# Performance work log

Measured on AMD Instinct MI355X. Metric: run time of the kernel, lower is better.

Reference implementation:

```python
import jax, jax.numpy as jnp
import numpy as np

N_CLS = 20
EMBED_DIM = 256


def setup_inputs() -> dict:
    key = jax.random.key(0)
    k1, k2 = jax.random.split(key)
    patch_embed = jax.random.normal(k1, (64, 4096, EMBED_DIM), dtype=jnp.float32)
    # xavier_uniform init for codebook: bound = sqrt(6/(fan_in+fan_out))
    bound = float(np.sqrt(6.0 / (N_CLS + EMBED_DIM)))
    codebook = jax.random.uniform(k2, (N_CLS, EMBED_DIM), dtype=jnp.float32,
                                  minval=-bound, maxval=bound)
    return {"patch_embed": patch_embed, "codebook": codebook}


def reference(patch_embed, codebook):
    # scores: (B, n_cls, N) = codebook (c,d) . patch_embed (b,n,d)
    attn = jnp.einsum('cd,bnd->bcn', codebook, patch_embed)
    attn = jax.nn.softmax(attn, axis=-1)
    # attn_patch: (B, n_cls, D)
    return jnp.einsum('bcn,bnd->bcd', attn, patch_embed)
```

## Files before the change

### kernel.cpp

```cpp
#include <hip/hip_runtime.h>
#include <cmath>

#define BATCH 64
#define NTOK  4096
#define DIM   256
#define NCLS  20
#define TILE  16
#define XPAD  65
#define CQ    17

#define GLOAD_LDS16(gp, lp) \
  __builtin_amdgcn_global_load_lds((const __attribute__((address_space(1))) void*)(gp), \
                                   (__attribute__((address_space(3))) void*)(lp), 16, 0, 0)

__device__ __forceinline__ float wave_sum64(float v) {
  #pragma unroll
  for (int m = 32; m >= 1; m >>= 1) v += __shfl_xor(v, m, 64);
  return v;
}

__global__ __launch_bounds__(256, 4) void patch_attn_chunk(
    const float* __restrict__ patch, const float* __restrict__ codebook,
    float* __restrict__ o_ws, float* __restrict__ l_ws, int nch) {
  __shared__ float4 Xs[TILE * XPAD];
  __shared__ float4 CBs[NCLS * 4 * CQ];
  __shared__ float4 Ps4[4 * TILE];
  __shared__ float  Ps1[4 * TILE];

  const int tid  = threadIdx.x;
  const int w    = tid >> 6;
  const int lane = tid & 63;
  const int r    = lane & 15;
  const int q    = lane >> 4;
  const int b    = blockIdx.x / nch;
  const int ch   = blockIdx.x - b * nch;
  const int rows = NTOK / nch;
  const int ntiles = rows / TILE;
  const float4* Xg  = (const float4*)patch + ((size_t)b * NTOK + (size_t)ch * rows) * (DIM / 4);
  const float4* cb4 = (const float4*)codebook;
  const int c0 = __builtin_amdgcn_readfirstlane(w * 5);

  #pragma unroll
  for (int idx = tid; idx < NCLS * 64; idx += 256) {
    int cls = idx >> 6, rest = idx & 63;
    int qq = rest >> 4, i = rest & 15;
    CBs[cls * (4 * CQ) + qq * CQ + i] = cb4[idx];
  }

  float4 o[5];
  float l_run[5];
  #pragma unroll
  for (int j = 0; j < 5; ++j) {
    o[j] = make_float4(0.f, 0.f, 0.f, 0.f);
    l_run[j] = 0.f;
  }

  for (int t = 0; t < ntiles; ++t) {
    const float4* srcT = Xg + (size_t)t * TILE * (DIM / 4);
    #pragma unroll
    for (int i = 0; i < 4; ++i) {
      const int n = i * 4 + w;
      GLOAD_LDS16(srcT + n * (DIM / 4) + lane, &Xs[n * XPAD + lane]);
    }
    __syncthreads();

    float s[5] = {0.f, 0.f, 0.f, 0.f, 0.f};
    {
      const int xb  = r * XPAD + q * 16;
      const int cbb = q * CQ;
      #pragma unroll 8
      for (int cbi = 0; cbi < 16; ++cbi) {
        float4 x = Xs[xb + cbi];
        #pragma unroll
        for (int j = 0; j < 5; ++j) {
          float4 cv = CBs[(c0 + j) * (4 * CQ) + cbb + cbi];
          s[j] = fmaf(x.x, cv.x, s[j]);
          s[j] = fmaf(x.y, cv.y, s[j]);
          s[j] = fmaf(x.z, cv.z, s[j]);
          s[j] = fmaf(x.w, cv.w, s[j]);
        }
      }
    }
    float p[5];
    #pragma unroll
    for (int j = 0; j < 5; ++j) {
      s[j] += __shfl_xor(s[j], 16, 64);
      s[j] += __shfl_xor(s[j], 32, 64);
      p[j] = __expf(s[j]);
      l_run[j] += p[j];
    }

    if (lane < 16) {
      Ps4[w * TILE + r] = make_float4(p[0], p[1], p[2], p[3]);
      Ps1[w * TILE + r] = p[4];
    }

    #pragma unroll 8
    for (int n = 0; n < TILE; ++n) {
      float4 x  = Xs[n * XPAD + lane];
      float4 pv = Ps4[w * TILE + n];
      float  p4 = Ps1[w * TILE + n];
      o[0].x = fmaf(pv.x, x.x, o[0].x); o[0].y = fmaf(pv.x, x.y, o[0].y);
      o[0].z = fmaf(pv.x, x.z, o[0].z); o[0].w = fmaf(pv.x, x.w, o[0].w);
      o[1].x = fmaf(pv.y, x.x, o[1].x); o[1].y = fmaf(pv.y, x.y, o[1].y);
      o[1].z = fmaf(pv.y, x.z, o[1].z); o[1].w = fmaf(pv.y, x.w, o[1].w);
      o[2].x = fmaf(pv.z, x.x, o[2].x); o[2].y = fmaf(pv.z, x.y, o[2].y);
      o[2].z = fmaf(pv.z, x.z, o[2].z); o[2].w = fmaf(pv.z, x.w, o[2].w);
      o[3].x = fmaf(pv.w, x.x, o[3].x); o[3].y = fmaf(pv.w, x.y, o[3].y);
      o[3].z = fmaf(pv.w, x.z, o[3].z); o[3].w = fmaf(pv.w, x.w, o[3].w);
      o[4].x = fmaf(p4,   x.x, o[4].x); o[4].y = fmaf(p4,   x.y, o[4].y);
      o[4].z = fmaf(p4,   x.z, o[4].z); o[4].w = fmaf(p4,   x.w, o[4].w);
    }
    __syncthreads();
  }

  const size_t base = (size_t)(b * nch + ch) * NCLS + c0;
  float4* og = (float4*)o_ws;
  #pragma unroll
  for (int j = 0; j < 5; ++j) og[(base + j) * (DIM / 4) + lane] = o[j];
  #pragma unroll
  for (int j = 0; j < 5; ++j) l_run[j] = 0.25f * wave_sum64(l_run[j]);
  if (lane == 0) {
    #pragma unroll
    for (int j = 0; j < 5; ++j) l_ws[base + j] = l_run[j];
  }
}

__global__ __launch_bounds__(256) void patch_attn_combine(
    const float* __restrict__ o_ws, const float* __restrict__ l_ws,
    float* __restrict__ out, int nch) {
  const int bc = blockIdx.x;
  const int b = bc / NCLS;
  const int c = bc - b * NCLS;
  const int d = threadIdx.x;

  float lg = 0.f, acc = 0.f;
  for (int ch = 0; ch < nch; ++ch) {
    size_t idx = ((size_t)b * nch + ch) * NCLS + c;
    lg  += l_ws[idx];
    acc += o_ws[idx * DIM + d];
  }
  out[(size_t)bc * DIM + d] = acc / lg;
}

extern "C" void kernel_launch(void* const* d_in, const int* in_sizes, int n_in,
                              void* d_out, int out_size, void* d_ws, size_t ws_size,
                              hipStream_t stream) {
  const float* patch = (const float*)d_in[0];
  const float* cbk   = (const float*)d_in[1];
  float* out = (float*)d_out;

  int nch = 16;
  while (nch > 1 && (size_t)BATCH * nch * NCLS * (DIM + 1) * sizeof(float) > ws_size) nch >>= 1;

  float* o_ws = (float*)d_ws;
  float* l_ws = o_ws + (size_t)BATCH * nch * NCLS * DIM;

  patch_attn_chunk<<<dim3(BATCH * nch), dim3(256), 0, stream>>>(patch, cbk, o_ws, l_ws, nch);
  patch_attn_combine<<<dim3(BATCH * NCLS), dim3(256), 0, stream>>>(o_ws, l_ws, out, nch);
}
```

Before: 390.1 us.

## Restructure chunk kernel with 64-row XOR-swizzled tiles and per-thread full-class accumulators

Grows the row tile from 16 to 64 and stores rows unpadded in LDS with an XOR swizzle to avoid bank conflicts. Each lane now computes full-dimension dot products for one row, reading codebook values straight from global memory, so the cross-lane shuffle reduction goes away. In the second GEMM each thread owns one output dimension and accumulates all 20 classes, with probabilities shared through LDS. The chunk count drops from 16 to 8 and occupancy is lowered to 2 blocks, trading register pressure and fewer barriers per row for fewer blocks in flight.

```diff
diff --git a/kernel.cpp b/kernel.cpp
--- a/kernel.cpp
+++ b/kernel.cpp
@@ -5,9 +5,7 @@
 #define NTOK  4096
 #define DIM   256
 #define NCLS  20
-#define TILE  16
-#define XPAD  65
-#define CQ    17
+#define RT    64
 
 #define GLOAD_LDS16(gp, lp) \
   __builtin_amdgcn_global_load_lds((const __attribute__((address_space(1))) void*)(gp), \
@@ -19,110 +17,116 @@
   return v;
 }
 
-__global__ __launch_bounds__(256, 4) void patch_attn_chunk(
+__global__ __launch_bounds__(256, 2) void patch_attn_chunk(
     const float* __restrict__ patch, const float* __restrict__ codebook,
     float* __restrict__ o_ws, float* __restrict__ l_ws, int nch) {
-  __shared__ float4 Xs[TILE * XPAD];
-  __shared__ float4 CBs[NCLS * 4 * CQ];
-  __shared__ float4 Ps4[4 * TILE];
-  __shared__ float  Ps1[4 * TILE];
+  __shared__ float4 Xs[RT * (DIM / 4)];
+  __shared__ float  Ps[RT * NCLS];
 
   const int tid  = threadIdx.x;
   const int w    = tid >> 6;
   const int lane = tid & 63;
-  const int r    = lane & 15;
-  const int q    = lane >> 4;
   const int b    = blockIdx.x / nch;
   const int ch   = blockIdx.x - b * nch;
   const int rows = NTOK / nch;
-  const int ntiles = rows / TILE;
+  const int ntiles = rows / RT;
   const float4* Xg  = (const float4*)patch + ((size_t)b * NTOK + (size_t)ch * rows) * (DIM / 4);
   const float4* cb4 = (const float4*)codebook;
   const int c0 = __builtin_amdgcn_readfirstlane(w * 5);
 
+  float o[NCLS];
   #pragma unroll
-  for (int idx = tid; idx < NCLS * 64; idx += 256) {
-    int cls = idx >> 6, rest = idx & 63;
-    int qq = rest >> 4, i = rest & 15;
-    CBs[cls * (4 * CQ) + qq * CQ + i] = cb4[idx];
-  }
+  for (int c = 0; c < NCLS; ++c) o[c] = 0.f;
+  float l0 = 0.f, l1 = 0.f, l2 = 0.f, l3 = 0.f, l4 = 0.f;
 
-  float4 o[5];
-  float l_run[5];
+  const int rx = lane & 7;
+  const float4* xp[8];
   #pragma unroll
-  for (int j = 0; j < 5; ++j) {
-    o[j] = make_float4(0.f, 0.f, 0.f, 0.f);
-    l_run[j] = 0.f;
-  }
+  for (int k = 0; k < 8; ++k) xp[k] = &Xs[lane * (DIM / 4) + (k ^ rx)];
+
+  const float* XsF = (const float*)Xs;
+  const int f4d = tid >> 2, fsub = tid & 3;
+  const float* xbp[8];
+  #pragma unroll
+  for (int k = 0; k < 8; ++k) xbp[k] = XsF + (k * DIM + ((f4d ^ k) << 2) + fsub);
 
   for (int t = 0; t < ntiles; ++t) {
-    const float4* srcT = Xg + (size_t)t * TILE * (DIM / 4);
+    const float4* srcT = Xg + (size_t)t * RT * (DIM / 4);
     #pragma unroll
-    for (int i = 0; i < 4; ++i) {
-      const int n = i * 4 + w;
-      GLOAD_LDS16(srcT + n * (DIM / 4) + lane, &Xs[n * XPAD + lane]);
+    for (int i = 0; i < 16; ++i) {
+      const int rr = w * 16 + i;
+      GLOAD_LDS16(srcT + rr * (DIM / 4) + (lane ^ (rr & 7)), &Xs[rr * (DIM / 4) + lane]);
     }
     __syncthreads();
 
-    float s[5] = {0.f, 0.f, 0.f, 0.f, 0.f};
     {
-      const int xb  = r * XPAD + q * 16;
-      const int cbb = q * CQ;
-      #pragma unroll 8
-      for (int cbi = 0; cbi < 16; ++cbi) {
-        float4 x = Xs[xb + cbi];
+      float s0 = 0.f, s1 = 0.f, s2 = 0.f, s3 = 0.f, s4 = 0.f;
+      #pragma unroll 2
+      for (int g = 0; g < 8; ++g) {
         #pragma unroll
-        for (int j = 0; j < 5; ++j) {
-          float4 cv = CBs[(c0 + j) * (4 * CQ) + cbb + cbi];
-          s[j] = fmaf(x.x, cv.x, s[j]);
-          s[j] = fmaf(x.y, cv.y, s[j]);
-          s[j] = fmaf(x.z, cv.z, s[j]);
-          s[j] = fmaf(x.w, cv.w, s[j]);
+        for (int k = 0; k < 8; ++k) {
+          const float4 x = xp[k][g * 8];
+          const int i = g * 8 + k;
+          const float4 ca = cb4[(c0 + 0) * (DIM / 4) + i];
+          const float4 cb = cb4[(c0 + 1) * (DIM / 4) + i];
+          const float4 cc = cb4[(c0 + 2) * (DIM / 4) + i];
+          const float4 cd = cb4[(c0 + 3) * (DIM / 4) + i];
+          const float4 ce = cb4[(c0 + 4) * (DIM / 4) + i];
+          s0 = fmaf(x.x, ca.x, s0); s0 = fmaf(x.y, ca.y, s0);
+          s0 = fmaf(x.z, ca.z, s0); s0 = fmaf(x.w, ca.w, s0);
+          s1 = fmaf(x.x, cb.x, s1); s1 = fmaf(x.y, cb.y, s1);
+          s1 = fmaf(x.z, cb.z, s1); s1 = fmaf(x.w, cb.w, s1);
+          s2 = fmaf(x.x, cc.x, s2); s2 = fmaf(x.y, cc.y, s2);
+          s2 = fmaf(x.z, cc.z, s2); s2 = fmaf(x.w, cc.w, s2);
+          s3 = fmaf(x.x, cd.x, s3); s3 = fmaf(x.y, cd.y, s3);
+          s3 = fmaf(x.z, cd.z, s3); s3 = fmaf(x.w, cd.w, s3);
+          s4 = fmaf(x.x, ce.x, s4); s4 = fmaf(x.y, ce.y, s4);
+          s4 = fmaf(x.z, ce.z, s4); s4 = fmaf(x.w, ce.w, s4);
         }
       }
+      const float p0 = __expf(s0), p1 = __expf(s1), p2 = __expf(s2),
+                  p3 = __expf(s3), p4 = __expf(s4);
+      l0 += p0; l1 += p1; l2 += p2; l3 += p3; l4 += p4;
+      float* psr = &Ps[lane * NCLS + c0];
+      psr[0] = p0; psr[1] = p1; psr[2] = p2; psr[3] = p3; psr[4] = p4;
     }
-    float p[5];
-    #pragma unroll
-    for (int j = 0; j < 5; ++j) {
-      s[j] += __shfl_xor(s[j], 16, 64);
-      s[j] += __shfl_xor(s[j], 32, 64);
-      p[j] = __expf(s[j]);
-      l_run[j] += p[j];
-    }
+    __syncthreads();
 
-    if (lane < 16) {
-      Ps4[w * TILE + r] = make_float4(p[0], p[1], p[2], p[3]);
-      Ps1[w * TILE + r] = p[4];
-    }
-
-    #pragma unroll 8
-    for (int n = 0; n < TILE; ++n) {
-      float4 x  = Xs[n * XPAD + lane];
-      float4 pv = Ps4[w * TILE + n];
-      float  p4 = Ps1[w * TILE + n];
-      o[0].x = fmaf(pv.x, x.x, o[0].x); o[0].y = fmaf(pv.x, x.y, o[0].y);
-      o[0].z = fmaf(pv.x, x.z, o[0].z); o[0].w = fmaf(pv.x, x.w, o[0].w);
-      o[1].x = fmaf(pv.y, x.x, o[1].x); o[1].y = fmaf(pv.y, x.y, o[1].y);
-      o[1].z = fmaf(pv.y, x.z, o[1].z); o[1].w = fmaf(pv.y, x.w, o[1].w);
-      o[2].x = fmaf(pv.z, x.x, o[2].x); o[2].y = fmaf(pv.z, x.y, o[2].y);
-      o[2].z = fmaf(pv.z, x.z, o[2].z); o[2].w = fmaf(pv.z, x.w, o[2].w);
-      o[3].x = fmaf(pv.w, x.x, o[3].x); o[3].y = fmaf(pv.w, x.y, o[3].y);
-      o[3].z = fmaf(pv.w, x.z, o[3].z); o[3].w = fmaf(pv.w, x.w, o[3].w);
-      o[4].x = fmaf(p4,   x.x, o[4].x); o[4].y = fmaf(p4,   x.y, o[4].y);
-      o[4].z = fmaf(p4,   x.z, o[4].z); o[4].w = fmaf(p4,   x.w, o[4].w);
+    #pragma unroll 2
+    for (int n0 = 0; n0 < RT; n0 += 8) {
+      #pragma unroll
+      for (int k = 0; k < 8; ++k) {
+        const int n = n0 + k;
+        const float x = xbp[k][n0 * DIM];
+        const float4 q0 = *(const float4*)&Ps[n * NCLS + 0];
+        const float4 q1 = *(const float4*)&Ps[n * NCLS + 4];
+        const float4 q2 = *(const float4*)&Ps[n * NCLS + 8];
+        const float4 q3 = *(const float4*)&Ps[n * NCLS + 12];
+        const float4 q4 = *(const float4*)&Ps[n * NCLS + 16];
+        o[0]  = fmaf(q0.x, x, o[0]);  o[1]  = fmaf(q0.y, x, o[1]);
+        o[2]  = fmaf(q0.z, x, o[2]);  o[3]  = fmaf(q0.w, x, o[3]);
+        o[4]  = fmaf(q1.x, x, o[4]);  o[5]  = fmaf(q1.y, x, o[5]);
+        o[6]  = fmaf(q1.z, x, o[6]);  o[7]  = fmaf(q1.w, x, o[7]);
+        o[8]  = fmaf(q2.x, x, o[8]);  o[9]  = fmaf(q2.y, x, o[9]);
+        o[10] = fmaf(q2.z, x, o[10]); o[11] = fmaf(q2.w, x, o[11]);
+        o[12] = fmaf(q3.x, x, o[12]); o[13] = fmaf(q3.y, x, o[13]);
+        o[14] = fmaf(q3.z, x, o[14]); o[15] = fmaf(q3.w, x, o[15]);
+        o[16] = fmaf(q4.x, x, o[16]); o[17] = fmaf(q4.y, x, o[17]);
+        o[18] = fmaf(q4.z, x, o[18]); o[19] = fmaf(q4.w, x, o[19]);
+      }
     }
     __syncthreads();
   }
 
-  const size_t base = (size_t)(b * nch + ch) * NCLS + c0;
-  float4* og = (float4*)o_ws;
+  const size_t base = (size_t)(b * nch + ch) * NCLS;
   #pragma unroll
-  for (int j = 0; j < 5; ++j) og[(base + j) * (DIM / 4) + lane] = o[j];
-  #pragma unroll
-  for (int j = 0; j < 5; ++j) l_run[j] = 0.25f * wave_sum64(l_run[j]);
+  for (int c = 0; c < NCLS; ++c) o_ws[(base + c) * DIM + tid] = o[c];
+  l0 = wave_sum64(l0); l1 = wave_sum64(l1); l2 = wave_sum64(l2);
+  l3 = wave_sum64(l3); l4 = wave_sum64(l4);
   if (lane == 0) {
-    #pragma unroll
-    for (int j = 0; j < 5; ++j) l_ws[base + j] = l_run[j];
+    l_ws[base + c0 + 0] = l0; l_ws[base + c0 + 1] = l1;
+    l_ws[base + c0 + 2] = l2; l_ws[base + c0 + 3] = l3;
+    l_ws[base + c0 + 4] = l4;
   }
 }
 
@@ -150,7 +154,7 @@
   const float* cbk   = (const float*)d_in[1];
   float* out = (float*)d_out;
 
-  int nch = 16;
+  int nch = 8;
   while (nch > 1 && (size_t)BATCH * nch * NCLS * (DIM + 1) * sizeof(float) > ws_size) nch >>= 1;
 
   float* o_ws = (float*)d_ws;
```

Measured after the change: 475.3 us. 1.22x slower.

## Restructure chunk kernel with 512-thread blocks, register-blocked scores and DPP reductions

Applied to the files above, without the earlier changes.

The chunk kernel now uses 512 threads in two row halves and loads a 32-row tile per step. Each wave computes scores for 4 rows by 5 classes with codebook values held in registers, and reduces across lanes with DPP row-shift adds instead of shuffles. The PV accumulation broadcasts probabilities with readlane instead of staging them through LDS. The LDS layout uses an XOR swizzle instead of padding, and the two half-block accumulators are merged through shared memory at the end. The chunk count is halved to 8, which gives fewer, larger blocks. The aim is fewer LDS accesses and less shuffle overhead, at the cost of more register pressure and lower block-level parallelism.

```diff
diff --git a/kernel.cpp b/kernel.cpp
--- a/kernel.cpp
+++ b/kernel.cpp
@@ -5,124 +5,160 @@
 #define NTOK  4096
 #define DIM   256
 #define NCLS  20
-#define TILE  16
-#define XPAD  65
-#define CQ    17
+#define RT    32
 
 #define GLOAD_LDS16(gp, lp) \
   __builtin_amdgcn_global_load_lds((const __attribute__((address_space(1))) void*)(gp), \
                                    (__attribute__((address_space(3))) void*)(lp), 16, 0, 0)
 
-__device__ __forceinline__ float wave_sum64(float v) {
-  #pragma unroll
-  for (int m = 32; m >= 1; m >>= 1) v += __shfl_xor(v, m, 64);
-  return v;
+#define DPP_SHR_ADD(v, N) \
+  v += __int_as_float(__builtin_amdgcn_update_dpp(0, __float_as_int(v), 0x110 | (N), 0xf, 0xf, true))
+
+__device__ __forceinline__ float rlane(float v, int srcl) {
+  return __int_as_float(__builtin_amdgcn_readlane(__float_as_int(v), srcl));
 }
 
-__global__ __launch_bounds__(256, 4) void patch_attn_chunk(
+__global__ __launch_bounds__(512, 4) void patch_attn_chunk(
     const float* __restrict__ patch, const float* __restrict__ codebook,
     float* __restrict__ o_ws, float* __restrict__ l_ws, int nch) {
-  __shared__ float4 Xs[TILE * XPAD];
-  __shared__ float4 CBs[NCLS * 4 * CQ];
-  __shared__ float4 Ps4[4 * TILE];
-  __shared__ float  Ps1[4 * TILE];
+  __shared__ float4 Xs[RT * (DIM / 4)];
+  __shared__ float4 CBs[NCLS * (DIM / 4)];
 
   const int tid  = threadIdx.x;
-  const int w    = tid >> 6;
   const int lane = tid & 63;
-  const int r    = lane & 15;
-  const int q    = lane >> 4;
+  const int uw   = __builtin_amdgcn_readfirstlane(tid >> 6);
+  const int g    = uw & 3;
+  const int rh   = uw >> 2;
+  const int r4   = lane >> 4;
+  const int k16  = lane & 15;
+  const int c0   = g * 5;
   const int b    = blockIdx.x / nch;
   const int ch   = blockIdx.x - b * nch;
   const int rows = NTOK / nch;
-  const int ntiles = rows / TILE;
+  const int ntiles = rows / RT;
   const float4* Xg  = (const float4*)patch + ((size_t)b * NTOK + (size_t)ch * rows) * (DIM / 4);
   const float4* cb4 = (const float4*)codebook;
-  const int c0 = __builtin_amdgcn_readfirstlane(w * 5);
 
+  for (int idx = tid; idx < NCLS * 64; idx += 512) CBs[idx] = cb4[idx];
+
+  const float4* xa[4];
   #pragma unroll
-  for (int idx = tid; idx < NCLS * 64; idx += 256) {
-    int cls = idx >> 6, rest = idx & 63;
-    int qq = rest >> 4, i = rest & 15;
-    CBs[cls * (4 * CQ) + qq * CQ + i] = cb4[idx];
+  for (int j = 0; j < 4; ++j) {
+    const int n = rh * 16 + r4 + 4 * j;
+    xa[j] = &Xs[n * 64 + (k16 & 8) + ((k16 & 7) ^ (n & 7))];
   }
+  const float4* cbp = &CBs[c0 * 64 + k16];
+
+  const int eA = lane & ~7, e = lane & 7;
 
   float4 o[5];
-  float l_run[5];
   #pragma unroll
-  for (int j = 0; j < 5; ++j) {
-    o[j] = make_float4(0.f, 0.f, 0.f, 0.f);
-    l_run[j] = 0.f;
-  }
+  for (int c = 0; c < 5; ++c) o[c] = make_float4(0.f, 0.f, 0.f, 0.f);
+  float l[5] = {0.f, 0.f, 0.f, 0.f, 0.f};
 
   for (int t = 0; t < ntiles; ++t) {
-    const float4* srcT = Xg + (size_t)t * TILE * (DIM / 4);
+    const float4* srcT = Xg + (size_t)t * RT * 64;
     #pragma unroll
     for (int i = 0; i < 4; ++i) {
-      const int n = i * 4 + w;
-      GLOAD_LDS16(srcT + n * (DIM / 4) + lane, &Xs[n * XPAD + lane]);
+      const int rr = uw * 4 + i;
+      GLOAD_LDS16(srcT + rr * 64 + (lane ^ (rr & 7)), &Xs[rr * 64 + lane]);
     }
     __syncthreads();
 
-    float s[5] = {0.f, 0.f, 0.f, 0.f, 0.f};
-    {
-      const int xb  = r * XPAD + q * 16;
-      const int cbb = q * CQ;
-      #pragma unroll 8
-      for (int cbi = 0; cbi < 16; ++cbi) {
-        float4 x = Xs[xb + cbi];
+    float s[4][5];
+    #pragma unroll
+    for (int j = 0; j < 4; ++j)
+      #pragma unroll
+      for (int c = 0; c < 5; ++c) s[j][c] = 0.f;
+
+    #pragma unroll
+    for (int mh = 0; mh < 2; ++mh) {
+      float4 cbr[5][2];
+      #pragma unroll
+      for (int c = 0; c < 5; ++c)
         #pragma unroll
-        for (int j = 0; j < 5; ++j) {
-          float4 cv = CBs[(c0 + j) * (4 * CQ) + cbb + cbi];
-          s[j] = fmaf(x.x, cv.x, s[j]);
-          s[j] = fmaf(x.y, cv.y, s[j]);
-          s[j] = fmaf(x.z, cv.z, s[j]);
-          s[j] = fmaf(x.w, cv.w, s[j]);
+        for (int mm = 0; mm < 2; ++mm)
+          cbr[c][mm] = cbp[c * 64 + (2 * mh + mm) * 16];
+      #pragma unroll
+      for (int j = 0; j < 4; ++j) {
+        #pragma unroll
+        for (int mm = 0; mm < 2; ++mm) {
+          const float4 x = xa[j][(2 * mh + mm) * 16];
+          #pragma unroll
+          for (int c = 0; c < 5; ++c) {
+            s[j][c] = fmaf(x.x, cbr[c][mm].x, s[j][c]);
+            s[j][c] = fmaf(x.y, cbr[c][mm].y, s[j][c]);
+            s[j][c] = fmaf(x.z, cbr[c][mm].z, s[j][c]);
+            s[j][c] = fmaf(x.w, cbr[c][mm].w, s[j][c]);
+          }
         }
       }
     }
-    float p[5];
+
+    float p[4][5];
     #pragma unroll
-    for (int j = 0; j < 5; ++j) {
-      s[j] += __shfl_xor(s[j], 16, 64);
-      s[j] += __shfl_xor(s[j], 32, 64);
-      p[j] = __expf(s[j]);
-      l_run[j] += p[j];
+    for (int j = 0; j < 4; ++j) {
+      #pragma unroll
+      for (int c = 0; c < 5; ++c) {
+        float v = s[j][c];
+        DPP_SHR_ADD(v, 1);
+        DPP_SHR_ADD(v, 2);
+        DPP_SHR_ADD(v, 4);
+        DPP_SHR_ADD(v, 8);
+        p[j][c] = __expf(v);
+      }
     }
 
-    if (lane < 16) {
-      Ps4[w * TILE + r] = make_float4(p[0], p[1], p[2], p[3]);
-      Ps1[w * TILE + r] = p[4];
-    }
-
-    #pragma unroll 8
-    for (int n = 0; n < TILE; ++n) {
-      float4 x  = Xs[n * XPAD + lane];
-      float4 pv = Ps4[w * TILE + n];
-      float  p4 = Ps1[w * TILE + n];
-      o[0].x = fmaf(pv.x, x.x, o[0].x); o[0].y = fmaf(pv.x, x.y, o[0].y);
-      o[0].z = fmaf(pv.x, x.z, o[0].z); o[0].w = fmaf(pv.x, x.w, o[0].w);
-      o[1].x = fmaf(pv.y, x.x, o[1].x); o[1].y = fmaf(pv.y, x.y, o[1].y);
-      o[1].z = fmaf(pv.y, x.z, o[1].z); o[1].w = fmaf(pv.y, x.w, o[1].w);
-      o[2].x = fmaf(pv.z, x.x, o[2].x); o[2].y = fmaf(pv.z, x.y, o[2].y);
-      o[2].z = fmaf(pv.z, x.z, o[2].z); o[2].w = fmaf(pv.z, x.w, o[2].w);
-      o[3].x = fmaf(pv.w, x.x, o[3].x); o[3].y = fmaf(pv.w, x.y, o[3].y);
-      o[3].z = fmaf(pv.w, x.z, o[3].z); o[3].w = fmaf(pv.w, x.w, o[3].w);
-      o[4].x = fmaf(p4,   x.x, o[4].x); o[4].y = fmaf(p4,   x.y, o[4].y);
-      o[4].z = fmaf(p4,   x.z, o[4].z); o[4].w = fmaf(p4,   x.w, o[4].w);
+    #pragma unroll
+    for (int r = 0; r < 16; ++r) {
+      const int n = rh * 16 + r;
+      const float4 x = Xs[n * 64 + eA + (e ^ (r & 7))];
+      const int sl = (r & 3) * 16 + 15;
+      const float q0 = rlane(p[r >> 2][0], sl);
+      const float q1 = rlane(p[r >> 2][1], sl);
+      const float q2 = rlane(p[r >> 2][2], sl);
+      const float q3 = rlane(p[r >> 2][3], sl);
+      const float q4 = rlane(p[r >> 2][4], sl);
+      o[0].x = fmaf(q0, x.x, o[0].x); o[0].y = fmaf(q0, x.y, o[0].y);
+      o[0].z = fmaf(q0, x.z, o[0].z); o[0].w = fmaf(q0, x.w, o[0].w);
+      o[1].x = fmaf(q1, x.x, o[1].x); o[1].y = fmaf(q1, x.y, o[1].y);
+      o[1].z = fmaf(q1, x.z, o[1].z); o[1].w = fmaf(q1, x.w, o[1].w);
+      o[2].x = fmaf(q2, x.x, o[2].x); o[2].y = fmaf(q2, x.y, o[2].y);
+      o[2].z = fmaf(q2, x.z, o[2].z); o[2].w = fmaf(q2, x.w, o[2].w);
+      o[3].x = fmaf(q3, x.x, o[3].x); o[3].y = fmaf(q3, x.y, o[3].y);
+      o[3].z = fmaf(q3, x.z, o[3].z); o[3].w = fmaf(q3, x.w, o[3].w);
+      o[4].x = fmaf(q4, x.x, o[4].x); o[4].y = fmaf(q4, x.y, o[4].y);
+      o[4].z = fmaf(q4, x.z, o[4].z); o[4].w = fmaf(q4, x.w, o[4].w);
+      l[0] += q0; l[1] += q1; l[2] += q2; l[3] += q3; l[4] += q4;
     }
     __syncthreads();
   }
 
-  const size_t base = (size_t)(b * nch + ch) * NCLS + c0;
-  float4* og = (float4*)o_ws;
-  #pragma unroll
-  for (int j = 0; j < 5; ++j) og[(base + j) * (DIM / 4) + lane] = o[j];
-  #pragma unroll
-  for (int j = 0; j < 5; ++j) l_run[j] = 0.25f * wave_sum64(l_run[j]);
-  if (lane == 0) {
+  float4* scr  = (float4*)Xs;
+  float*  scrL = (float*)Xs + 20 * 256;
+  if (rh) {
     #pragma unroll
-    for (int j = 0; j < 5; ++j) l_ws[base + j] = l_run[j];
+    for (int c = 0; c < 5; ++c) scr[(c0 + c) * 64 + lane] = o[c];
+    if (lane == 0) {
+      #pragma unroll
+      for (int c = 0; c < 5; ++c) scrL[c0 + c] = l[c];
+    }
+  }
+  __syncthreads();
+  if (!rh) {
+    const size_t base = (size_t)(b * nch + ch) * NCLS;
+    float4* og = (float4*)o_ws;
+    #pragma unroll
+    for (int c = 0; c < 5; ++c) {
+      const float4 m = scr[(c0 + c) * 64 + lane];
+      float4 v = o[c];
+      v.x += m.x; v.y += m.y; v.z += m.z; v.w += m.w;
+      og[(base + c0 + c) * 64 + lane] = v;
+    }
+    if (lane == 0) {
+      #pragma unroll
+      for (int c = 0; c < 5; ++c) l_ws[base + c0 + c] = l[c] + scrL[c0 + c];
+    }
   }
 }
 
@@ -150,12 +186,12 @@
   const float* cbk   = (const float*)d_in[1];
   float* out = (float*)d_out;
 
-  int nch = 16;
+  int nch = 8;
   while (nch > 1 && (size_t)BATCH * nch * NCLS * (DIM + 1) * sizeof(float) > ws_size) nch >>= 1;
 
   float* o_ws = (float*)d_ws;
   float* l_ws = o_ws + (size_t)BATCH * nch * NCLS * DIM;
 
-  patch_attn_chunk<<<dim3(BATCH * nch), dim3(256), 0, stream>>>(patch, cbk, o_ws, l_ws, nch);
+  patch_attn_chunk<<<dim3(BATCH * nch), dim3(512), 0, stream>>>(patch, cbk, o_ws, l_ws, nch);
   patch_attn_combine<<<dim3(BATCH * NCLS), dim3(256), 0, stream>>>(o_ws, l_ws, out, nch);
 }
```

Result: faster. 379.1 us (-2.8%).
